# Kernel tuning notes

Hardware: AMD Instinct MI355X
Metric: run time of the kernel (lower is better)

Reference implementation:

```python
import jax, jax.numpy as jnp
import numpy as np
import math

ANSWER_LEN = 11
D_MODEL = 6
MAX_SEQ_LEN = 34
POS_DIM = 3
TOK_DIM = 3
HEAD_DIM = 3
N_HEADS = 2
FFN_DIM = 6
VOCAB_SIZE = 14
B = 65536
T = 34
EPS = 1e-5


def setup_inputs() -> dict:
    key = jax.random.key(0)
    ks = jax.random.split(key, 16)
    s = 0.1
    return {
        "idx": jax.random.randint(ks[0], (B, T), 0, VOCAB_SIZE, dtype=jnp.int32),
        "tok_emb": jax.random.normal(ks[1], (VOCAB_SIZE, TOK_DIM), jnp.float32) * s,
        "pos_enc": jax.random.normal(ks[2], (MAX_SEQ_LEN, POS_DIM), jnp.float32) * s,
        "wq": jax.random.normal(ks[3], (POS_DIM, N_HEADS * HEAD_DIM), jnp.float32) * s,
        "wk": jax.random.normal(ks[4], (POS_DIM, N_HEADS * HEAD_DIM), jnp.float32) * s,
        "wv": jax.random.normal(ks[5], (TOK_DIM, N_HEADS * HEAD_DIM), jnp.float32) * s,
        "wo": jax.random.normal(ks[6], (N_HEADS * HEAD_DIM, D_MODEL), jnp.float32) * s,
        "ln1_g": jnp.ones((D_MODEL,), jnp.float32),
        "ln1_b": jnp.zeros((D_MODEL,), jnp.float32),
        "ln2_g": jnp.ones((D_MODEL,), jnp.float32),
        "ln2_b": jnp.zeros((D_MODEL,), jnp.float32),
        "w1": jax.random.normal(ks[7], (D_MODEL, FFN_DIM), jnp.float32) * s,
        "b1": jnp.zeros((FFN_DIM,), jnp.float32),
        "w2": jax.random.normal(ks[8], (FFN_DIM, D_MODEL), jnp.float32) * s,
        "b2": jnp.zeros((D_MODEL,), jnp.float32),
        "lnf_g": jnp.ones((D_MODEL,), jnp.float32),
        "lnf_b": jnp.zeros((D_MODEL,), jnp.float32),
        "w_head": jax.random.normal(ks[9], (D_MODEL, VOCAB_SIZE), jnp.float32) * s,
    }


def _layernorm(x, g, b):
    mu = jnp.mean(x, axis=-1, keepdims=True)
    var = jnp.var(x, axis=-1, keepdims=True)
    return (x - mu) * jax.lax.rsqrt(var + EPS) * g + b


def _attn(x, wq, wk, wv, wo):
    Bt, Tt, _ = x.shape
    x_tok = x[:, :, :TOK_DIM]   # [B,T,3]
    x_pos = x[:, :, TOK_DIM:]   # [B,T,3]
    q = (x_pos @ wq).reshape(Bt, Tt, N_HEADS, HEAD_DIM)
    k = (x_pos @ wk).reshape(Bt, Tt, N_HEADS, HEAD_DIM)
    v = (x_tok @ wv).reshape(Bt, Tt, N_HEADS, HEAD_DIM)
    scores = jnp.einsum('bqhd,bkhd->bhqk', q, k) / math.sqrt(HEAD_DIM)
    causal = jnp.tril(jnp.ones((Tt, Tt), bool))
    scores = jnp.where(causal, scores, -jnp.inf)
    attn = jax.nn.softmax(scores, axis=-1)
    out = jnp.einsum('bhqk,bkhd->bqhd', attn, v).reshape(Bt, Tt, N_HEADS * HEAD_DIM)
    return out @ wo


def reference(idx, tok_emb, pos_enc, wq, wk, wv, wo, ln1_g, ln1_b, ln2_g, ln2_b,
              w1, b1, w2, b2, lnf_g, lnf_b, w_head):
    Bt, Tt = idx.shape
    tok = tok_emb[idx]                                   # [B,T,3]
    pos = jnp.broadcast_to(pos_enc[:Tt][None], (Bt, Tt, POS_DIM))
    x = jnp.concatenate([tok, pos], axis=-1)             # [B,T,6]
    x = x + _attn(_layernorm(x, ln1_g, ln1_b), wq, wk, wv, wo)
    h = _layernorm(x, ln2_g, ln2_b)
    x = x + (jax.nn.gelu(h @ w1 + b1, approximate=False) @ w2 + b2)
    x = _layernorm(x, lnf_g, lnf_b)
    return x @ w_head                                    # [B,T,VOCAB]
```

## Files before the change

kernel.cpp:

```cpp
#include <hip/hip_runtime.h>
#include <math.h>

#define B_SEQ 65536
#define T_SEQ 34
#define VOCAB 14
#define NTOK (B_SEQ * T_SEQ)
#define NBLK 8704

__device__ __forceinline__ void layernorm6(const float* x, const float* g,
                                           const float* bt, float* o) {
    float mu = (x[0] + x[1] + x[2] + x[3] + x[4] + x[5]) * (1.0f / 6.0f);
    float var = 0.0f;
#pragma unroll
    for (int i = 0; i < 6; ++i) { float d = x[i] - mu; var += d * d; }
    var *= (1.0f / 6.0f);
    float rs = rsqrtf(var + 1e-5f);
#pragma unroll
    for (int i = 0; i < 6; ++i) o[i] = (x[i] - mu) * rs * g[i] + bt[i];
}

__global__ __launch_bounds__(256) void fused_tf_kernel(
    const int* __restrict__ idx,
    const float* __restrict__ tok_emb,
    const float* __restrict__ pos_enc,
    const float* __restrict__ wq,
    const float* __restrict__ wk,
    const float* __restrict__ wv,
    const float* __restrict__ wo,
    const float* __restrict__ ln1_g, const float* __restrict__ ln1_b,
    const float* __restrict__ ln2_g, const float* __restrict__ ln2_b,
    const float* __restrict__ w1,   const float* __restrict__ b1,
    const float* __restrict__ w2,   const float* __restrict__ b2,
    const float* __restrict__ lnf_g, const float* __restrict__ lnf_b,
    const float* __restrict__ w_head,
    float* __restrict__ out)
{
    __shared__ float kvtab[T_SEQ * VOCAB * 12];

    const int tid = threadIdx.x;

    for (int e = tid; e < T_SEQ * VOCAB; e += 256) {
        const int t = e / VOCAB;
        const int v = e - t * VOCAB;
        float x[6];
#pragma unroll
        for (int i = 0; i < 3; ++i) x[i] = tok_emb[v * 3 + i];
#pragma unroll
        for (int i = 0; i < 3; ++i) x[3 + i] = pos_enc[t * 3 + i];
        float xl[6];
        layernorm6(x, ln1_g, ln1_b, xl);
        float* dst = &kvtab[e * 12];
#pragma unroll
        for (int j = 0; j < 6; ++j) {
            dst[j]     = xl[3] * wk[j] + xl[4] * wk[6 + j] + xl[5] * wk[12 + j];
            dst[6 + j] = xl[0] * wv[j] + xl[1] * wv[6 + j] + xl[2] * wv[12 + j];
        }
    }
    __syncthreads();

    const int g = blockIdx.x * 256 + tid;
    const unsigned b = (unsigned)g / (unsigned)T_SEQ;
    const int t = g - (int)b * T_SEQ;

    const int mytok = idx[g];
    float x[6];
#pragma unroll
    for (int i = 0; i < 3; ++i) x[i] = tok_emb[mytok * 3 + i];
#pragma unroll
    for (int i = 0; i < 3; ++i) x[3 + i] = pos_enc[t * 3 + i];
    float xl[6];
    layernorm6(x, ln1_g, ln1_b, xl);
    float q[6];
    const float scale = 0.57735026918962576f;
#pragma unroll
    for (int j = 0; j < 6; ++j)
        q[j] = (xl[3] * wq[j] + xl[4] * wq[6 + j] + xl[5] * wq[12 + j]) * scale;

    float den0 = 0.0f, den1 = 0.0f;
    float acc[6] = {0.f, 0.f, 0.f, 0.f, 0.f, 0.f};
    const int base = (int)b * T_SEQ;
    for (int s = 0; s <= t; ++s) {
        const int tk = idx[base + s];
        const float* e = &kvtab[(s * VOCAB + tk) * 12];
        const float s0 = q[0] * e[0] + q[1] * e[1] + q[2] * e[2];
        const float s1 = q[3] * e[3] + q[4] * e[4] + q[5] * e[5];
        const float p0 = __expf(s0);
        const float p1 = __expf(s1);
        den0 += p0; den1 += p1;
        acc[0] += p0 * e[6];  acc[1] += p0 * e[7];  acc[2] += p0 * e[8];
        acc[3] += p1 * e[9];  acc[4] += p1 * e[10]; acc[5] += p1 * e[11];
    }
    const float inv0 = 1.0f / den0;
    const float inv1 = 1.0f / den1;
    float ao[6];
#pragma unroll
    for (int i = 0; i < 3; ++i) { ao[i] = acc[i] * inv0; ao[3 + i] = acc[3 + i] * inv1; }

    float x2[6];
#pragma unroll
    for (int j = 0; j < 6; ++j) {
        float s = x[j];
#pragma unroll
        for (int i = 0; i < 6; ++i) s += ao[i] * wo[i * 6 + j];
        x2[j] = s;
    }

    float h[6];
    layernorm6(x2, ln2_g, ln2_b, h);
    float f[6];
#pragma unroll
    for (int j = 0; j < 6; ++j) {
        float s = b1[j];
#pragma unroll
        for (int i = 0; i < 6; ++i) s += h[i] * w1[i * 6 + j];
        f[j] = 0.5f * s * (1.0f + erff(s * 0.70710678118654752f));
    }
    float x3[6];
#pragma unroll
    for (int j = 0; j < 6; ++j) {
        float s = x2[j] + b2[j];
#pragma unroll
        for (int i = 0; i < 6; ++i) s += f[i] * w2[i * 6 + j];
        x3[j] = s;
    }

    float xo[6];
    layernorm6(x3, lnf_g, lnf_b, xo);
    float o[14];
#pragma unroll
    for (int j = 0; j < 14; ++j) {
        float s = 0.0f;
#pragma unroll
        for (int i = 0; i < 6; ++i) s += xo[i] * w_head[i * 14 + j];
        o[j] = s;
    }

    float2* op = (float2*)(out + (size_t)g * 14);
#pragma unroll
    for (int j = 0; j < 7; ++j) op[j] = make_float2(o[2 * j], o[2 * j + 1]);
}

extern "C" void kernel_launch(void* const* d_in, const int* in_sizes, int n_in,
                              void* d_out, int out_size, void* d_ws, size_t ws_size,
                              hipStream_t stream) {
    const int*   idx     = (const int*)d_in[0];
    const float* tok_emb = (const float*)d_in[1];
    const float* pos_enc = (const float*)d_in[2];
    const float* wq      = (const float*)d_in[3];
    const float* wk      = (const float*)d_in[4];
    const float* wv      = (const float*)d_in[5];
    const float* wo      = (const float*)d_in[6];
    const float* ln1_g   = (const float*)d_in[7];
    const float* ln1_b   = (const float*)d_in[8];
    const float* ln2_g   = (const float*)d_in[9];
    const float* ln2_b   = (const float*)d_in[10];
    const float* w1      = (const float*)d_in[11];
    const float* b1      = (const float*)d_in[12];
    const float* w2      = (const float*)d_in[13];
    const float* b2      = (const float*)d_in[14];
    const float* lnf_g   = (const float*)d_in[15];
    const float* lnf_b   = (const float*)d_in[16];
    const float* w_head  = (const float*)d_in[17];
    float* out = (float*)d_out;

    hipLaunchKernelGGL(fused_tf_kernel, dim3(NBLK), dim3(256), 0, stream,
                       idx, tok_emb, pos_enc, wq, wk, wv, wo,
                       ln1_g, ln1_b, ln2_g, ln2_b, w1, b1, w2, b2,
                       lnf_g, lnf_b, w_head, out);
}
```

Before: 230.4 us.

## Remap threads to sequence-major layout with LDS-staged indices and vectorized KV reads

Each block now handles 16 whole sequences with 576 threads. Threads are mapped so a wavefront holds the same position across different sequences, which balances causal loop lengths inside each wavefront. Token indices are staged once in shared memory instead of being re-read from global memory inside the attention loop, and KV table entries are read as float4. Each block also builds the KV table in a single pass. The tradeoffs are 32 idle threads per block (576 minus 544 active) and scattered output writes, since adjacent threads now write to different sequences.

```diff
diff --git a/kernel.cpp b/kernel.cpp
--- a/kernel.cpp
+++ b/kernel.cpp
@@ -4,8 +4,10 @@
 #define B_SEQ 65536
 #define T_SEQ 34
 #define VOCAB 14
-#define NTOK (B_SEQ * T_SEQ)
-#define NBLK 8704
+#define SEQS_PER_BLK 16
+#define ACTIVE (SEQS_PER_BLK * T_SEQ)
+#define BLK_THREADS 576
+#define NBLK (B_SEQ / SEQS_PER_BLK)
 
 __device__ __forceinline__ void layernorm6(const float* x, const float* g,
                                            const float* bt, float* o) {
@@ -19,7 +21,7 @@
     for (int i = 0; i < 6; ++i) o[i] = (x[i] - mu) * rs * g[i] + bt[i];
 }
 
-__global__ __launch_bounds__(256) void fused_tf_kernel(
+__global__ __launch_bounds__(BLK_THREADS) void fused_tf_kernel(
     const int* __restrict__ idx,
     const float* __restrict__ tok_emb,
     const float* __restrict__ pos_enc,
@@ -35,11 +37,13 @@
     const float* __restrict__ w_head,
     float* __restrict__ out)
 {
-    __shared__ float kvtab[T_SEQ * VOCAB * 12];
+    __shared__ __align__(16) float kvtab[T_SEQ * VOCAB * 12];
+    __shared__ int idx_lds[ACTIVE];
 
     const int tid = threadIdx.x;
 
-    for (int e = tid; e < T_SEQ * VOCAB; e += 256) {
+    if (tid < T_SEQ * VOCAB) {
+        const int e = tid;
         const int t = e / VOCAB;
         const int v = e - t * VOCAB;
         float x[6];
@@ -56,13 +60,18 @@
             dst[6 + j] = xl[0] * wv[j] + xl[1] * wv[6 + j] + xl[2] * wv[12 + j];
         }
     }
+    if (tid < ACTIVE) idx_lds[tid] = idx[blockIdx.x * ACTIVE + tid];
     __syncthreads();
 
-    const int g = blockIdx.x * 256 + tid;
-    const unsigned b = (unsigned)g / (unsigned)T_SEQ;
-    const int t = g - (int)b * T_SEQ;
+    if (tid >= ACTIVE) return;
 
-    const int mytok = idx[g];
+    const int seq = tid & 15;
+    const int t   = 33 - (tid >> 4);
+    const int b   = blockIdx.x * SEQS_PER_BLK + seq;
+    const int g   = b * T_SEQ + t;
+    const int* myidx = &idx_lds[seq * T_SEQ];
+
+    const int mytok = myidx[t];
     float x[6];
 #pragma unroll
     for (int i = 0; i < 3; ++i) x[i] = tok_emb[mytok * 3 + i];
@@ -78,17 +87,19 @@
 
     float den0 = 0.0f, den1 = 0.0f;
     float acc[6] = {0.f, 0.f, 0.f, 0.f, 0.f, 0.f};
-    const int base = (int)b * T_SEQ;
     for (int s = 0; s <= t; ++s) {
-        const int tk = idx[base + s];
-        const float* e = &kvtab[(s * VOCAB + tk) * 12];
-        const float s0 = q[0] * e[0] + q[1] * e[1] + q[2] * e[2];
-        const float s1 = q[3] * e[3] + q[4] * e[4] + q[5] * e[5];
+        const int tk = myidx[s];
+        const float4* e4 = (const float4*)&kvtab[(s * VOCAB + tk) * 12];
+        const float4 ea = e4[0];
+        const float4 eb = e4[1];
+        const float4 ec = e4[2];
+        const float s0 = q[0] * ea.x + q[1] * ea.y + q[2] * ea.z;
+        const float s1 = q[3] * ea.w + q[4] * eb.x + q[5] * eb.y;
         const float p0 = __expf(s0);
         const float p1 = __expf(s1);
         den0 += p0; den1 += p1;
-        acc[0] += p0 * e[6];  acc[1] += p0 * e[7];  acc[2] += p0 * e[8];
-        acc[3] += p1 * e[9];  acc[4] += p1 * e[10]; acc[5] += p1 * e[11];
+        acc[0] += p0 * eb.z;  acc[1] += p0 * eb.w;  acc[2] += p0 * ec.x;
+        acc[3] += p1 * ec.y;  acc[4] += p1 * ec.z;  acc[5] += p1 * ec.w;
     }
     const float inv0 = 1.0f / den0;
     const float inv1 = 1.0f / den1;
@@ -163,7 +174,7 @@
     const float* w_head  = (const float*)d_in[17];
     float* out = (float*)d_out;
 
-    hipLaunchKernelGGL(fused_tf_kernel, dim3(NBLK), dim3(256), 0, stream,
+    hipLaunchKernelGGL(fused_tf_kernel, dim3(NBLK), dim3(BLK_THREADS), 0, stream,
                        idx, tok_emb, pos_enc, wq, wk, wv, wo,
                        ln1_g, ln1_b, ln2_g, ln2_b, w1, b1, w2, b2,
                        lnf_g, lnf_b, w_head, out);
```

Result: no change. 225.9 us (-1.9%).

## Register-block query rows per thread and precompute Q/K/V tables in shared memory

Applied to the files above, without the earlier changes.

Each block now handles 64 whole sequences with 576 threads. Each thread owns 4 (or 2) consecutive query positions of one sequence, so every K/V table entry it loads is reused across several queries. The Q projection and the embeddings are precomputed per (position, token) into shared memory as float4/float2 arrays. Token offsets are staged in padded shared memory, and exp is replaced by exp2 with log2e folded into the K scale. This cuts redundant global idx reads, shared-memory loads and per-token projection work, in exchange for more registers, uneven work across the row groups and higher shared-memory use per block.

```diff
diff --git a/kernel.cpp b/kernel.cpp
--- a/kernel.cpp
+++ b/kernel.cpp
@@ -1,11 +1,13 @@
 #include <hip/hip_runtime.h>
 #include <math.h>
 
-#define B_SEQ 65536
 #define T_SEQ 34
 #define VOCAB 14
-#define NTOK (B_SEQ * T_SEQ)
-#define NBLK 8704
+#define NE (T_SEQ * VOCAB)
+#define SEQS 64
+#define BLK 576
+#define NBLK 1024
+#define OFFP 35
 
 __device__ __forceinline__ void layernorm6(const float* x, const float* g,
                                            const float* bt, float* o) {
@@ -19,7 +21,114 @@
     for (int i = 0; i < 6; ++i) o[i] = (x[i] - mu) * rs * g[i] + bt[i];
 }
 
-__global__ __launch_bounds__(256) void fused_tf_kernel(
+template <int NT>
+__device__ __forceinline__ void run_rows(
+    int T0, int seq, int blk,
+    const float4* __restrict__ kvA, const float4* __restrict__ kvB,
+    const float4* __restrict__ kvC,
+    const float4* __restrict__ qA,  const float2* __restrict__ qB,
+    const float4* __restrict__ xA,  const float2* __restrict__ xB,
+    const int* __restrict__ myoff,
+    const float* __restrict__ wo,
+    const float* __restrict__ ln2_g, const float* __restrict__ ln2_b,
+    const float* __restrict__ w1,   const float* __restrict__ b1,
+    const float* __restrict__ w2,   const float* __restrict__ b2,
+    const float* __restrict__ lnf_g, const float* __restrict__ lnf_b,
+    const float* __restrict__ w_head,
+    float* __restrict__ out)
+{
+    float q[NT][6];
+#pragma unroll
+    for (int i = 0; i < NT; ++i) {
+        const int e = myoff[T0 + i];
+        const float4 a = qA[e]; const float2 b2v = qB[e];
+        q[i][0] = a.x; q[i][1] = a.y; q[i][2] = a.z;
+        q[i][3] = a.w; q[i][4] = b2v.x; q[i][5] = b2v.y;
+    }
+    float den0[NT], den1[NT], acc[NT][6];
+#pragma unroll
+    for (int i = 0; i < NT; ++i) {
+        den0[i] = 0.f; den1[i] = 0.f;
+#pragma unroll
+        for (int j = 0; j < 6; ++j) acc[i][j] = 0.f;
+    }
+
+    auto body = [&](int e, int imin) {
+        const float4 ea = kvA[e], eb = kvB[e], ec = kvC[e];
+#pragma unroll
+        for (int i = 0; i < NT; ++i) {
+            if (i >= imin) {
+                const float s0 = q[i][0] * ea.x + q[i][1] * ea.y + q[i][2] * ea.z;
+                const float s1 = q[i][3] * ea.w + q[i][4] * eb.x + q[i][5] * eb.y;
+                const float p0 = exp2f(s0);
+                const float p1 = exp2f(s1);
+                den0[i] += p0; den1[i] += p1;
+                acc[i][0] += p0 * eb.z; acc[i][1] += p0 * eb.w; acc[i][2] += p0 * ec.x;
+                acc[i][3] += p1 * ec.y; acc[i][4] += p1 * ec.z; acc[i][5] += p1 * ec.w;
+            }
+        }
+    };
+
+    for (int s = 0; s < T0; ++s) body(myoff[s], 0);
+#pragma unroll
+    for (int j = 0; j < NT; ++j) body(myoff[T0 + j], j);
+
+#pragma unroll
+    for (int i = 0; i < NT; ++i) {
+        const int t = T0 + i;
+        const int e = myoff[t];
+        const float inv0 = __builtin_amdgcn_rcpf(den0[i]);
+        const float inv1 = __builtin_amdgcn_rcpf(den1[i]);
+        float ao[6];
+#pragma unroll
+        for (int d = 0; d < 3; ++d) { ao[d] = acc[i][d] * inv0; ao[3 + d] = acc[i][3 + d] * inv1; }
+        const float4 xa = xA[e]; const float2 xb = xB[e];
+        const float x[6] = {xa.x, xa.y, xa.z, xa.w, xb.x, xb.y};
+        float x2[6];
+#pragma unroll
+        for (int j = 0; j < 6; ++j) {
+            float s = x[j];
+#pragma unroll
+            for (int k = 0; k < 6; ++k) s += ao[k] * wo[k * 6 + j];
+            x2[j] = s;
+        }
+        float h[6];
+        layernorm6(x2, ln2_g, ln2_b, h);
+        float f[6];
+#pragma unroll
+        for (int j = 0; j < 6; ++j) {
+            float s = b1[j];
+#pragma unroll
+            for (int k = 0; k < 6; ++k) s += h[k] * w1[k * 6 + j];
+            f[j] = 0.5f * s * (1.0f + erff(s * 0.70710678118654752f));
+        }
+        float x3[6];
+#pragma unroll
+        for (int j = 0; j < 6; ++j) {
+            float s = x2[j] + b2[j];
+#pragma unroll
+            for (int k = 0; k < 6; ++k) s += f[k] * w2[k * 6 + j];
+            x3[j] = s;
+        }
+        float xo[6];
+        layernorm6(x3, lnf_g, lnf_b, xo);
+
+        const size_t g = ((size_t)(blk * SEQS + seq)) * T_SEQ + t;
+        float2* op = (float2*)(out + g * 14);
+#pragma unroll
+        for (int jj = 0; jj < 7; ++jj) {
+            float o0 = 0.f, o1 = 0.f;
+#pragma unroll
+            for (int k = 0; k < 6; ++k) {
+                o0 += xo[k] * w_head[k * 14 + 2 * jj];
+                o1 += xo[k] * w_head[k * 14 + 2 * jj + 1];
+            }
+            op[jj] = make_float2(o0, o1);
+        }
+    }
+}
+
+__global__ __launch_bounds__(BLK, 5) void fused_tf_kernel(
     const int* __restrict__ idx,
     const float* __restrict__ tok_emb,
     const float* __restrict__ pos_enc,
@@ -35,13 +144,27 @@
     const float* __restrict__ w_head,
     float* __restrict__ out)
 {
-    __shared__ float kvtab[T_SEQ * VOCAB * 12];
+    __shared__ float4 kvA[NE];
+    __shared__ float4 kvB[NE];
+    __shared__ float4 kvC[NE];
+    __shared__ float4 qA[NE];
+    __shared__ float2 qB[NE];
+    __shared__ float4 xA[NE];
+    __shared__ float2 xB[NE];
+    __shared__ int offt[SEQS * OFFP];
 
     const int tid = threadIdx.x;
 
-    for (int e = tid; e < T_SEQ * VOCAB; e += 256) {
-        const int t = e / VOCAB;
-        const int v = e - t * VOCAB;
+    for (int i = tid; i < SEQS * T_SEQ; i += BLK) {
+        const int sq = i / T_SEQ;
+        const int s  = i - sq * T_SEQ;
+        const int tok = idx[(size_t)blockIdx.x * (SEQS * T_SEQ) + i];
+        offt[sq * OFFP + s] = s * VOCAB + tok;
+    }
+
+    if (tid < NE) {
+        const int t = tid / VOCAB;
+        const int v = tid - t * VOCAB;
         float x[6];
 #pragma unroll
         for (int i = 0; i < 3; ++i) x[i] = tok_emb[v * 3 + i];
@@ -49,95 +172,36 @@
         for (int i = 0; i < 3; ++i) x[3 + i] = pos_enc[t * 3 + i];
         float xl[6];
         layernorm6(x, ln1_g, ln1_b, xl);
-        float* dst = &kvtab[e * 12];
-#pragma unroll
-        for (int j = 0; j < 6; ++j) {
-            dst[j]     = xl[3] * wk[j] + xl[4] * wk[6 + j] + xl[5] * wk[12 + j];
-            dst[6 + j] = xl[0] * wv[j] + xl[1] * wv[6 + j] + xl[2] * wv[12 + j];
-        }
+        const float kscale = 0.8329812666744317f;
+        float qv[6], kv6[6], vv[6];
+#pragma unroll
+        for (int j = 0; j < 6; ++j) {
+            qv[j]  =  xl[3] * wq[j] + xl[4] * wq[6 + j] + xl[5] * wq[12 + j];
+            kv6[j] = (xl[3] * wk[j] + xl[4] * wk[6 + j] + xl[5] * wk[12 + j]) * kscale;
+            vv[j]  =  xl[0] * wv[j] + xl[1] * wv[6 + j] + xl[2] * wv[12 + j];
+        }
+        kvA[tid] = make_float4(kv6[0], kv6[1], kv6[2], kv6[3]);
+        kvB[tid] = make_float4(kv6[4], kv6[5], vv[0], vv[1]);
+        kvC[tid] = make_float4(vv[2], vv[3], vv[4], vv[5]);
+        qA[tid]  = make_float4(qv[0], qv[1], qv[2], qv[3]);
+        qB[tid]  = make_float2(qv[4], qv[5]);
+        xA[tid]  = make_float4(x[0], x[1], x[2], x[3]);
+        xB[tid]  = make_float2(x[4], x[5]);
     }
     __syncthreads();
 
-    const int g = blockIdx.x * 256 + tid;
-    const unsigned b = (unsigned)g / (unsigned)T_SEQ;
-    const int t = g - (int)b * T_SEQ;
-
-    const int mytok = idx[g];
-    float x[6];
-#pragma unroll
-    for (int i = 0; i < 3; ++i) x[i] = tok_emb[mytok * 3 + i];
-#pragma unroll
-    for (int i = 0; i < 3; ++i) x[3 + i] = pos_enc[t * 3 + i];
-    float xl[6];
-    layernorm6(x, ln1_g, ln1_b, xl);
-    float q[6];
-    const float scale = 0.57735026918962576f;
-#pragma unroll
-    for (int j = 0; j < 6; ++j)
-        q[j] = (xl[3] * wq[j] + xl[4] * wq[6 + j] + xl[5] * wq[12 + j]) * scale;
-
-    float den0 = 0.0f, den1 = 0.0f;
-    float acc[6] = {0.f, 0.f, 0.f, 0.f, 0.f, 0.f};
-    const int base = (int)b * T_SEQ;
-    for (int s = 0; s <= t; ++s) {
-        const int tk = idx[base + s];
-        const float* e = &kvtab[(s * VOCAB + tk) * 12];
-        const float s0 = q[0] * e[0] + q[1] * e[1] + q[2] * e[2];
-        const float s1 = q[3] * e[3] + q[4] * e[4] + q[5] * e[5];
-        const float p0 = __expf(s0);
-        const float p1 = __expf(s1);
-        den0 += p0; den1 += p1;
-        acc[0] += p0 * e[6];  acc[1] += p0 * e[7];  acc[2] += p0 * e[8];
-        acc[3] += p1 * e[9];  acc[4] += p1 * e[10]; acc[5] += p1 * e[11];
-    }
-    const float inv0 = 1.0f / den0;
-    const float inv1 = 1.0f / den1;
-    float ao[6];
-#pragma unroll
-    for (int i = 0; i < 3; ++i) { ao[i] = acc[i] * inv0; ao[3 + i] = acc[3 + i] * inv1; }
-
-    float x2[6];
-#pragma unroll
-    for (int j = 0; j < 6; ++j) {
-        float s = x[j];
-#pragma unroll
-        for (int i = 0; i < 6; ++i) s += ao[i] * wo[i * 6 + j];
-        x2[j] = s;
-    }
-
-    float h[6];
-    layernorm6(x2, ln2_g, ln2_b, h);
-    float f[6];
-#pragma unroll
-    for (int j = 0; j < 6; ++j) {
-        float s = b1[j];
-#pragma unroll
-        for (int i = 0; i < 6; ++i) s += h[i] * w1[i * 6 + j];
-        f[j] = 0.5f * s * (1.0f + erff(s * 0.70710678118654752f));
-    }
-    float x3[6];
-#pragma unroll
-    for (int j = 0; j < 6; ++j) {
-        float s = x2[j] + b2[j];
-#pragma unroll
-        for (int i = 0; i < 6; ++i) s += f[i] * w2[i * 6 + j];
-        x3[j] = s;
-    }
-
-    float xo[6];
-    layernorm6(x3, lnf_g, lnf_b, xo);
-    float o[14];
-#pragma unroll
-    for (int j = 0; j < 14; ++j) {
-        float s = 0.0f;
-#pragma unroll
-        for (int i = 0; i < 6; ++i) s += xo[i] * w_head[i * 14 + j];
-        o[j] = s;
-    }
-
-    float2* op = (float2*)(out + (size_t)g * 14);
-#pragma unroll
-    for (int j = 0; j < 7; ++j) op[j] = make_float2(o[2 * j], o[2 * j + 1]);
+    const int seq = tid & 63;
+    const int grp = tid >> 6;
+    const int* myoff = &offt[seq * OFFP];
+
+    if (grp < 8)
+        run_rows<4>(4 * grp, seq, blockIdx.x, kvA, kvB, kvC, qA, qB, xA, xB,
+                    myoff, wo, ln2_g, ln2_b, w1, b1, w2, b2, lnf_g, lnf_b,
+                    w_head, out);
+    else
+        run_rows<2>(32, seq, blockIdx.x, kvA, kvB, kvC, qA, qB, xA, xB,
+                    myoff, wo, ln2_g, ln2_b, w1, b1, w2, b2, lnf_g, lnf_b,
+                    w_head, out);
 }
 
 extern "C" void kernel_launch(void* const* d_in, const int* in_sizes, int n_in,
@@ -163,7 +227,7 @@
     const float* w_head  = (const float*)d_in[17];
     float* out = (float*)d_out;
 
-    hipLaunchKernelGGL(fused_tf_kernel, dim3(NBLK), dim3(256), 0, stream,
+    hipLaunchKernelGGL(fused_tf_kernel, dim3(NBLK), dim3(BLK), 0, stream,
                        idx, tok_emb, pos_enc, wq, wk, wv, wo,
                        ln1_g, ln1_b, ln2_g, ln2_b, w1, b1, w2, b2,
                        lnf_g, lnf_b, w_head, out);
```

Result: slower. 277.3 us (+20.3%).
